# Performance work log

Measured on AMD Instinct MI355X. Metric: run time of the kernel, lower is better.

## Reference

```python
import jax, jax.numpy as jnp
import numpy as np

D_MODEL = 1024
D_HEAD = 64
M_BITS = 32


def setup_inputs() -> dict:
    key = jax.random.key(0)
    ks = jax.random.split(key, 6)
    B, N, M = 2, 2048, 2048
    Q = jax.random.normal(ks[0], (B, N, D_MODEL), dtype=jnp.float32)
    K = jax.random.normal(ks[1], (B, M, D_MODEL), dtype=jnp.float32)
    V = jax.random.normal(ks[2], (B, M, D_MODEL), dtype=jnp.float32)
    s = 1.0 / np.sqrt(D_MODEL)
    Wq = jax.random.normal(ks[3], (D_MODEL, M_BITS), dtype=jnp.float32) * s
    Wk = jax.random.normal(ks[4], (D_MODEL, M_BITS), dtype=jnp.float32) * s
    Wv = jax.random.normal(ks[5], (D_MODEL, D_HEAD), dtype=jnp.float32) * s
    temperature = jnp.ones((1,), dtype=jnp.float32)
    return {"Q": Q, "K": K, "V": V, "Wq": Wq, "Wk": Wk, "Wv": Wv,
            "temperature": temperature}


def tropical_matmul(A, Bt):
    # A: [B, N, m], Bt: [B, M, m] (already transposed form of [B, m, M])
    # (A \odot B)_{ij} = min_k (A_ik + B_kj)
    return jnp.min(A[:, :, None, :] + Bt[:, None, :, :], axis=-1)  # [B, N, M]


def reference(Q, K, V, Wq, Wk, Wv, temperature):
    # REWA tropical encoders (continuous): linear projections to m_bits
    Qt = jnp.einsum('bnd,dm->bnm', Q, Wq)   # [B, N, m_bits]
    Kt = jnp.einsum('bsd,dm->bsm', K, Wk)   # [B, M, m_bits]
    Vp = jnp.einsum('bsd,dh->bsh', V, Wv)   # [B, M, d_head]
    # tropical (min-plus) scores, negated so shorter paths score higher
    scores = -tropical_matmul(Qt, Kt)       # [B, N, M]
    scores = scores / jax.nn.softplus(temperature[0])
    attn = jax.nn.softmax(scores, axis=-1)  # [B, N, M]
    out = jnp.einsum('bnm,bmh->bnh', attn, Vp)  # [B, N, d_head]
    return out, attn
```

## Files before the change

### kernel.cpp

```cpp
#include <hip/hip_runtime.h>
#include <math.h>

#define DM 1024
#define NB 2048
#define MBITS 32
#define DH 64

typedef __attribute__((ext_vector_type(4))) float floatx4;
typedef __attribute__((ext_vector_type(8))) short shortx8;

__device__ __forceinline__ unsigned short f32_to_bf16(float f) {
    union { float f; unsigned u; } v; v.f = f;
    unsigned r = v.u + 0x7FFF + ((v.u >> 16) & 1);
    return (unsigned short)(r >> 16);
}

__device__ __forceinline__ void split2(float x0, float x1, unsigned& hp, unsigned& lp) {
    union { float f; unsigned u; } a, b; a.f = x0; b.f = x1;
    unsigned h0 = a.u & 0xFFFF0000u, h1 = b.u & 0xFFFF0000u;
    union { unsigned u; float f; } hf0, hf1; hf0.u = h0; hf1.u = h1;
    union { float f; unsigned u; } c, d;
    c.f = x0 - hf0.f;
    d.f = x1 - hf1.f;
    hp = (h0 >> 16) | h1;
    lp = (c.u >> 16) | (d.u & 0xFFFF0000u);
}

__global__ __launch_bounds__(256) void wprep_kernel(
    const float* __restrict__ Wq, const float* __restrict__ Wk,
    const float* __restrict__ Wv, unsigned short* __restrict__ Wf)
{
    int wv = blockIdx.x * 4 + (threadIdx.x >> 6);
    int l  = threadIdx.x & 63;
    const float* W; int C, kc32, ct;
    if (wv < 64)       { W = Wq; C = 32; kc32 = wv >> 1;  ct = wv & 1; }
    else if (wv < 128) { W = Wk; C = 32; int z = wv - 64;  kc32 = z >> 1; ct = z & 1; }
    else               { W = Wv; C = 64; int z = wv - 128; kc32 = z >> 2; ct = z & 3; }
    int k0 = kc32 * 32 + (l >> 4) * 8;
    int c  = ct * 16 + (l & 15);
    float x[8];
    #pragma unroll
    for (int j = 0; j < 8; ++j) x[j] = W[(size_t)(k0 + j) * C + c];
    unsigned hp[4], lp[4];
    #pragma unroll
    for (int j2 = 0; j2 < 4; ++j2) split2(x[2 * j2], x[2 * j2 + 1], hp[j2], lp[j2]);
    uint4 hv; hv.x = hp[0]; hv.y = hp[1]; hv.z = hp[2]; hv.w = hp[3];
    uint4 lv; lv.x = lp[0]; lv.y = lp[1]; lv.z = lp[2]; lv.w = lp[3];
    *(uint4*)&Wf[(size_t)wv * 1024 + l * 8]       = hv;
    *(uint4*)&Wf[(size_t)wv * 1024 + 512 + l * 8] = lv;
}

__global__ __launch_bounds__(256) void proj_mfma2_kernel(
    const float* __restrict__ Q, const float* __restrict__ K, const float* __restrict__ V,
    const unsigned short* __restrict__ Wf,
    float* __restrict__ Qt, float* __restrict__ Kt, unsigned short* __restrict__ VpT)
{
    __shared__ float red[4][64][16];

    int gb = blockIdx.x;
    int job = gb >> 8, tile = gb & 255;
    int r0 = tile * 16;
    const float* X = (job == 0) ? Q : (job == 1) ? K : V;
    int ntct  = (job == 2) ? 4 : 2;
    int pbase = job << 6;
    int t = threadIdx.x, w = t >> 6, l = t & 63;
    int lrow = l & 15, lq = l >> 4;

    const float* xrow = &X[(size_t)(r0 + lrow) * DM + w * 256 + lq * 8];

    floatx4 acc[4];
    #pragma unroll
    for (int i = 0; i < 4; ++i) acc[i] = (floatx4){0.f, 0.f, 0.f, 0.f};

    floatx4 g0 = *(const floatx4*)(xrow);
    floatx4 g1 = *(const floatx4*)(xrow + 4);

    #pragma unroll
    for (int s = 0; s < 8; ++s) {
        floatx4 n0, n1;
        if (s < 7) {
            n0 = *(const floatx4*)(xrow + (s + 1) * 32);
            n1 = *(const floatx4*)(xrow + (s + 1) * 32 + 4);
        }
        union { unsigned u[4]; shortx8 v; } ahi, alo;
        split2(g0.x, g0.y, ahi.u[0], alo.u[0]);
        split2(g0.z, g0.w, ahi.u[1], alo.u[1]);
        split2(g1.x, g1.y, ahi.u[2], alo.u[2]);
        split2(g1.z, g1.w, ahi.u[3], alo.u[3]);
        int kc32 = w * 8 + s;
        #pragma unroll
        for (int ct = 0; ct < 4; ++ct) {
            if (ct >= ntct) break;
            int p = pbase + kc32 * ntct + ct;
            const unsigned short* wp = &Wf[(size_t)p * 1024 + l * 8];
            shortx8 bhi = *(const shortx8*)wp;
            shortx8 blo = *(const shortx8*)(wp + 512);
            acc[ct] = __builtin_amdgcn_mfma_f32_16x16x32_bf16(ahi.v, bhi, acc[ct], 0, 0, 0);
            acc[ct] = __builtin_amdgcn_mfma_f32_16x16x32_bf16(ahi.v, blo, acc[ct], 0, 0, 0);
            acc[ct] = __builtin_amdgcn_mfma_f32_16x16x32_bf16(alo.v, bhi, acc[ct], 0, 0, 0);
        }
        g0 = n0; g1 = n1;
    }

    #pragma unroll
    for (int ct = 0; ct < 4; ++ct) {
        if (ct >= ntct) break;
        #pragma unroll
        for (int r = 0; r < 4; ++r) red[w][l][ct * 4 + r] = acc[ct][r];
    }
    __syncthreads();

    int row = r0 + lq * 4 + w;
    if (job < 2) {
        float* Y = (job == 0) ? Qt : Kt;
        #pragma unroll
        for (int ct = 0; ct < 2; ++ct) {
            float v = red[0][l][ct * 4 + w] + red[1][l][ct * 4 + w]
                    + red[2][l][ct * 4 + w] + red[3][l][ct * 4 + w];
            Y[(size_t)row * MBITS + ct * 16 + lrow] = v;
        }
    } else {
        int b = row >> 11, j = row & 2047;
        #pragma unroll
        for (int ct = 0; ct < 4; ++ct) {
            float v = red[0][l][ct * 4 + w] + red[1][l][ct * 4 + w]
                    + red[2][l][ct * 4 + w] + red[3][l][ct * 4 + w];
            VpT[(size_t)b * (DH * NB) + (size_t)(ct * 16 + lrow) * NB + j] = f32_to_bf16(v);
        }
    }
}

__global__ __launch_bounds__(256) void trop_sum_kernel(
    const float* __restrict__ Qt, const float* __restrict__ Kt,
    const float* __restrict__ temp, float* __restrict__ partial)
{
    __shared__ float Qs[16][36];
    __shared__ float Ks[256][36];

    int b  = blockIdx.z;
    int jc = blockIdx.y;
    int i0 = blockIdx.x * 16;
    int t  = threadIdx.x;
    int w  = t >> 6, l = t & 63;

    if (t < 128) {
        int row = t >> 3, k4 = t & 7;
        *(floatx4*)&Qs[row][k4 * 4] =
            *(const floatx4*)&Qt[(size_t)(b * NB + i0 + row) * MBITS + k4 * 4];
    }
    #pragma unroll
    for (int u = 0; u < 8; ++u) {
        int flat4 = u * 256 + t;
        int row = flat4 >> 3, k4 = flat4 & 7;
        *(floatx4*)&Ks[row][k4 * 4] =
            *(const floatx4*)&Kt[(size_t)(b * NB + jc * 256 + row) * MBITS + k4 * 4];
    }
    float tv = temp[0];
    float c2 = -(1.0f / log1pf(__expf(tv))) * 1.44269504088896340736f;
    __syncthreads();

    float m[4][4];
    #pragma unroll
    for (int ii = 0; ii < 4; ++ii)
        #pragma unroll
        for (int jj = 0; jj < 4; ++jj) m[ii][jj] = 1e30f;

    #pragma unroll
    for (int k4 = 0; k4 < 8; ++k4) {
        floatx4 q[4], kk[4];
        #pragma unroll
        for (int ii = 0; ii < 4; ++ii) q[ii] = *(const floatx4*)&Qs[w + 4 * ii][k4 * 4];
        #pragma unroll
        for (int jj = 0; jj < 4; ++jj) kk[jj] = *(const floatx4*)&Ks[l + 64 * jj][k4 * 4];
        #pragma unroll
        for (int ii = 0; ii < 4; ++ii)
            #pragma unroll
            for (int jj = 0; jj < 4; ++jj) {
                float a0 = q[ii].x + kk[jj].x;
                float a1 = q[ii].y + kk[jj].y;
                float a2 = q[ii].z + kk[jj].z;
                float a3 = q[ii].w + kk[jj].w;
                m[ii][jj] = fminf(fminf(m[ii][jj], fminf(a0, a1)), fminf(a2, a3));
            }
    }

    #pragma unroll
    for (int ii = 0; ii < 4; ++ii) {
        float s = exp2f(c2 * m[ii][0]) + exp2f(c2 * m[ii][1])
                + exp2f(c2 * m[ii][2]) + exp2f(c2 * m[ii][3]);
        #pragma unroll
        for (int off = 1; off < 64; off <<= 1) s += __shfl_xor(s, off, 64);
        if (l == 0) partial[((size_t)b * NB + i0 + w + 4 * ii) * 8 + jc] = s;
    }
}

__global__ __launch_bounds__(256) void trop_fused_kernel(
    const float* __restrict__ Qt, const float* __restrict__ Kt,
    const unsigned short* __restrict__ VpT,
    const float* __restrict__ temp, const float* __restrict__ partial,
    float* __restrict__ outp, float* __restrict__ attn)
{
    __shared__ float Qs[16][36];
    __shared__ float Ks[256][36];
    __shared__ unsigned short Es[16][264];
    __shared__ float inv_s[16];

    int b  = blockIdx.z;
    int jc = blockIdx.y;
    int i0 = blockIdx.x * 16;
    int t  = threadIdx.x;
    int w  = t >> 6, l = t & 63;

    if (t < 128) {
        int row = t >> 3, k4 = t & 7;
        *(floatx4*)&Qs[row][k4 * 4] =
            *(const floatx4*)&Qt[(size_t)(b * NB + i0 + row) * MBITS + k4 * 4];
    }
    #pragma unroll
    for (int u = 0; u < 8; ++u) {
        int flat4 = u * 256 + t;
        int row = flat4 >> 3, k4 = flat4 & 7;
        *(floatx4*)&Ks[row][k4 * 4] =
            *(const floatx4*)&Kt[(size_t)(b * NB + jc * 256 + row) * MBITS + k4 * 4];
    }
    if (t < 16) {
        float s = 0.f;
        #pragma unroll
        for (int p = 0; p < 8; ++p) s += partial[((size_t)b * NB + i0 + t) * 8 + p];
        inv_s[t] = 1.0f / s;
    }
    float tv = temp[0];
    float c2 = -(1.0f / log1pf(__expf(tv))) * 1.44269504088896340736f;
    __syncthreads();

    float m[4][4];
    #pragma unroll
    for (int ii = 0; ii < 4; ++ii)
        #pragma unroll
        for (int jj = 0; jj < 4; ++jj) m[ii][jj] = 1e30f;

    #pragma unroll
    for (int k4 = 0; k4 < 8; ++k4) {
        floatx4 q[4], kk[4];
        #pragma unroll
        for (int ii = 0; ii < 4; ++ii) q[ii] = *(const floatx4*)&Qs[w + 4 * ii][k4 * 4];
        #pragma unroll
        for (int jj = 0; jj < 4; ++jj) kk[jj] = *(const floatx4*)&Ks[l + 64 * jj][k4 * 4];
        #pragma unroll
        for (int ii = 0; ii < 4; ++ii)
            #pragma unroll
            for (int jj = 0; jj < 4; ++jj) {
                float a0 = q[ii].x + kk[jj].x;
                float a1 = q[ii].y + kk[jj].y;
                float a2 = q[ii].z + kk[jj].z;
                float a3 = q[ii].w + kk[jj].w;
                m[ii][jj] = fminf(fminf(m[ii][jj], fminf(a0, a1)), fminf(a2, a3));
            }
    }

    #pragma unroll
    for (int ii = 0; ii < 4; ++ii) {
        int i = w + 4 * ii;
        float iv = inv_s[i];
        #pragma unroll
        for (int jj = 0; jj < 4; ++jj) {
            int j = l + 64 * jj;
            float e = exp2f(c2 * m[ii][jj]);
            attn[(size_t)(b * NB + i0 + i) * 2048 + jc * 256 + j] = e * iv;
            Es[i][j] = f32_to_bf16(e);
        }
    }
    __syncthreads();

    const unsigned short* vb =
        &VpT[(size_t)b * (DH * NB) + (size_t)(w * 16 + (l & 15)) * NB
             + jc * 256 + (l >> 4) * 8];
    floatx4 acc = {0.f, 0.f, 0.f, 0.f};
    #pragma unroll
    for (int kk = 0; kk < 8; ++kk) {
        int mrow = l & 15, q4 = l >> 4;
        shortx8 a  = *(const shortx8*)&Es[mrow][kk * 32 + q4 * 8];
        shortx8 bf = *(const shortx8*)(vb + kk * 32);
        acc = __builtin_amdgcn_mfma_f32_16x16x32_bf16(a, bf, acc, 0, 0, 0);
    }

    #pragma unroll
    for (int r = 0; r < 4; ++r) {
        int irow = (l >> 4) * 4 + r;
        atomicAdd(&outp[(size_t)(b * NB + i0 + irow) * DH + w * 16 + (l & 15)],
                  acc[r] * inv_s[irow]);
    }
}

extern "C" void kernel_launch(void* const* d_in, const int* in_sizes, int n_in,
                              void* d_out, int out_size, void* d_ws, size_t ws_size,
                              hipStream_t stream) {
    (void)in_sizes; (void)n_in; (void)out_size; (void)ws_size;
    const float* Q    = (const float*)d_in[0];
    const float* K    = (const float*)d_in[1];
    const float* V    = (const float*)d_in[2];
    const float* Wq   = (const float*)d_in[3];
    const float* Wk   = (const float*)d_in[4];
    const float* Wv   = (const float*)d_in[5];
    const float* temp = (const float*)d_in[6];

    float* outp = (float*)d_out;
    float* attn = outp + 2 * 2048 * 64;

    char* ws = (char*)d_ws;
    float*          Qt      = (float*)(ws);
    float*          Kt      = (float*)(ws + 524288);
    float*          partial = (float*)(ws + 1048576);
    unsigned short* Wf      = (unsigned short*)(ws + 1179648);
    unsigned short* VpT     = (unsigned short*)(ws + 1703936);

    hipMemsetAsync(d_out, 0, 262144 * sizeof(float), stream);

    wprep_kernel<<<64, 256, 0, stream>>>(Wq, Wk, Wv, Wf);
    proj_mfma2_kernel<<<768, 256, 0, stream>>>(Q, K, V, Wf, Qt, Kt, VpT);
    trop_sum_kernel<<<dim3(128, 8, 2), 256, 0, stream>>>(Qt, Kt, temp, partial);
    trop_fused_kernel<<<dim3(128, 8, 2), 256, 0, stream>>>(
        Qt, Kt, VpT, temp, partial, outp, attn);
}
```

Before: 161.2 us.

## Split projection K over 8 waves, swizzle K tiles, replace atomics with partial reduce

The projection kernel now runs 512 threads, with 8 waves each covering half as much of the K dimension, and templates the column-tile count so the inner loop has no branch. In the tropical kernels the padded LDS rows become XOR-swizzled rows, the min chain is rewritten, and the fused kernel reuses the K buffer for the exp tile to cut LDS use. The output atomics and the memset are replaced by per-chunk partial stores plus a separate reduction kernel. The changes trade an extra launch and extra workspace traffic against less contention and better occupancy.

```diff
diff --git a/kernel.cpp b/kernel.cpp
--- a/kernel.cpp
+++ b/kernel.cpp
@@ -50,12 +50,46 @@
     *(uint4*)&Wf[(size_t)wv * 1024 + 512 + l * 8] = lv;
 }
 
-__global__ __launch_bounds__(256) void proj_mfma2_kernel(
+template <int NTCT>
+__device__ __forceinline__ void proj_core(
+    const float* xrow, const unsigned short* __restrict__ Wf,
+    int pbase, int kc32base, int l, floatx4 acc[4])
+{
+    floatx4 g0 = *(const floatx4*)(xrow);
+    floatx4 g1 = *(const floatx4*)(xrow + 4);
+    #pragma unroll
+    for (int s = 0; s < 4; ++s) {
+        floatx4 n0, n1;
+        if (s < 3) {
+            n0 = *(const floatx4*)(xrow + (s + 1) * 32);
+            n1 = *(const floatx4*)(xrow + (s + 1) * 32 + 4);
+        }
+        union { unsigned u[4]; shortx8 v; } ahi, alo;
+        split2(g0.x, g0.y, ahi.u[0], alo.u[0]);
+        split2(g0.z, g0.w, ahi.u[1], alo.u[1]);
+        split2(g1.x, g1.y, ahi.u[2], alo.u[2]);
+        split2(g1.z, g1.w, ahi.u[3], alo.u[3]);
+        int kc32 = kc32base + s;
+        #pragma unroll
+        for (int ct = 0; ct < NTCT; ++ct) {
+            int p = pbase + kc32 * NTCT + ct;
+            const unsigned short* wp = &Wf[(size_t)p * 1024 + l * 8];
+            shortx8 bhi = *(const shortx8*)wp;
+            shortx8 blo = *(const shortx8*)(wp + 512);
+            acc[ct] = __builtin_amdgcn_mfma_f32_16x16x32_bf16(ahi.v, bhi, acc[ct], 0, 0, 0);
+            acc[ct] = __builtin_amdgcn_mfma_f32_16x16x32_bf16(ahi.v, blo, acc[ct], 0, 0, 0);
+            acc[ct] = __builtin_amdgcn_mfma_f32_16x16x32_bf16(alo.v, bhi, acc[ct], 0, 0, 0);
+        }
+        g0 = n0; g1 = n1;
+    }
+}
+
+__global__ __launch_bounds__(512) void proj_mfma3_kernel(
     const float* __restrict__ Q, const float* __restrict__ K, const float* __restrict__ V,
     const unsigned short* __restrict__ Wf,
     float* __restrict__ Qt, float* __restrict__ Kt, unsigned short* __restrict__ VpT)
 {
-    __shared__ float red[4][64][16];
+    __shared__ float red[8][64][17];
 
     int gb = blockIdx.x;
     int job = gb >> 8, tile = gb & 255;
@@ -66,41 +100,14 @@
     int t = threadIdx.x, w = t >> 6, l = t & 63;
     int lrow = l & 15, lq = l >> 4;
 
-    const float* xrow = &X[(size_t)(r0 + lrow) * DM + w * 256 + lq * 8];
+    const float* xrow = &X[(size_t)(r0 + lrow) * DM + w * 128 + lq * 8];
 
     floatx4 acc[4];
     #pragma unroll
     for (int i = 0; i < 4; ++i) acc[i] = (floatx4){0.f, 0.f, 0.f, 0.f};
 
-    floatx4 g0 = *(const floatx4*)(xrow);
-    floatx4 g1 = *(const floatx4*)(xrow + 4);
-
-    #pragma unroll
-    for (int s = 0; s < 8; ++s) {
-        floatx4 n0, n1;
-        if (s < 7) {
-            n0 = *(const floatx4*)(xrow + (s + 1) * 32);
-            n1 = *(const floatx4*)(xrow + (s + 1) * 32 + 4);
-        }
-        union { unsigned u[4]; shortx8 v; } ahi, alo;
-        split2(g0.x, g0.y, ahi.u[0], alo.u[0]);
-        split2(g0.z, g0.w, ahi.u[1], alo.u[1]);
-        split2(g1.x, g1.y, ahi.u[2], alo.u[2]);
-        split2(g1.z, g1.w, ahi.u[3], alo.u[3]);
-        int kc32 = w * 8 + s;
-        #pragma unroll
-        for (int ct = 0; ct < 4; ++ct) {
-            if (ct >= ntct) break;
-            int p = pbase + kc32 * ntct + ct;
-            const unsigned short* wp = &Wf[(size_t)p * 1024 + l * 8];
-            shortx8 bhi = *(const shortx8*)wp;
-            shortx8 blo = *(const shortx8*)(wp + 512);
-            acc[ct] = __builtin_amdgcn_mfma_f32_16x16x32_bf16(ahi.v, bhi, acc[ct], 0, 0, 0);
-            acc[ct] = __builtin_amdgcn_mfma_f32_16x16x32_bf16(ahi.v, blo, acc[ct], 0, 0, 0);
-            acc[ct] = __builtin_amdgcn_mfma_f32_16x16x32_bf16(alo.v, bhi, acc[ct], 0, 0, 0);
-        }
-        g0 = n0; g1 = n1;
-    }
+    if (job < 2) proj_core<2>(xrow, Wf, pbase, w * 4, l, acc);
+    else         proj_core<4>(xrow, Wf, pbase, w * 4, l, acc);
 
     #pragma unroll
     for (int ct = 0; ct < 4; ++ct) {
@@ -110,22 +117,26 @@
     }
     __syncthreads();
 
-    int row = r0 + lq * 4 + w;
-    if (job < 2) {
-        float* Y = (job == 0) ? Qt : Kt;
-        #pragma unroll
-        for (int ct = 0; ct < 2; ++ct) {
-            float v = red[0][l][ct * 4 + w] + red[1][l][ct * 4 + w]
-                    + red[2][l][ct * 4 + w] + red[3][l][ct * 4 + w];
-            Y[(size_t)row * MBITS + ct * 16 + lrow] = v;
-        }
-    } else {
-        int b = row >> 11, j = row & 2047;
-        #pragma unroll
-        for (int ct = 0; ct < 4; ++ct) {
-            float v = red[0][l][ct * 4 + w] + red[1][l][ct * 4 + w]
-                    + red[2][l][ct * 4 + w] + red[3][l][ct * 4 + w];
-            VpT[(size_t)b * (DH * NB) + (size_t)(ct * 16 + lrow) * NB + j] = f32_to_bf16(v);
+    if (w < 4) {
+        int row = r0 + lq * 4 + w;
+        if (job < 2) {
+            float* Y = (job == 0) ? Qt : Kt;
+            #pragma unroll
+            for (int ct = 0; ct < 2; ++ct) {
+                float v = 0.f;
+                #pragma unroll
+                for (int s = 0; s < 8; ++s) v += red[s][l][ct * 4 + w];
+                Y[(size_t)row * MBITS + ct * 16 + lrow] = v;
+            }
+        } else {
+            int b = row >> 11, j = row & 2047;
+            #pragma unroll
+            for (int ct = 0; ct < 4; ++ct) {
+                float v = 0.f;
+                #pragma unroll
+                for (int s = 0; s < 8; ++s) v += red[s][l][ct * 4 + w];
+                VpT[(size_t)b * (DH * NB) + (size_t)(ct * 16 + lrow) * NB + j] = f32_to_bf16(v);
+            }
         }
     }
 }
@@ -134,8 +145,8 @@
     const float* __restrict__ Qt, const float* __restrict__ Kt,
     const float* __restrict__ temp, float* __restrict__ partial)
 {
-    __shared__ float Qs[16][36];
-    __shared__ float Ks[256][36];
+    __shared__ float Qs[16][32];
+    __shared__ float Ks[256][32];
 
     int b  = blockIdx.z;
     int jc = blockIdx.y;
@@ -144,16 +155,16 @@
     int w  = t >> 6, l = t & 63;
 
     if (t < 128) {
-        int row = t >> 3, k4 = t & 7;
-        *(floatx4*)&Qs[row][k4 * 4] =
-            *(const floatx4*)&Qt[(size_t)(b * NB + i0 + row) * MBITS + k4 * 4];
+        int row = t >> 3, c4 = t & 7;
+        *(floatx4*)&Qs[row][c4 * 4] =
+            *(const floatx4*)&Qt[(size_t)(b * NB + i0 + row) * MBITS + c4 * 4];
     }
     #pragma unroll
     for (int u = 0; u < 8; ++u) {
         int flat4 = u * 256 + t;
-        int row = flat4 >> 3, k4 = flat4 & 7;
-        *(floatx4*)&Ks[row][k4 * 4] =
-            *(const floatx4*)&Kt[(size_t)(b * NB + jc * 256 + row) * MBITS + k4 * 4];
+        int row = flat4 >> 3, c4 = flat4 & 7;
+        *(floatx4*)&Ks[row][(c4 ^ (row & 7)) * 4] =
+            *(const floatx4*)&Kt[(size_t)(b * NB + jc * 256 + row) * MBITS + c4 * 4];
     }
     float tv = temp[0];
     float c2 = -(1.0f / log1pf(__expf(tv))) * 1.44269504088896340736f;
@@ -165,22 +176,21 @@
         #pragma unroll
         for (int jj = 0; jj < 4; ++jj) m[ii][jj] = 1e30f;
 
+    int swz = l & 7;
     #pragma unroll
     for (int k4 = 0; k4 < 8; ++k4) {
         floatx4 q[4], kk[4];
         #pragma unroll
         for (int ii = 0; ii < 4; ++ii) q[ii] = *(const floatx4*)&Qs[w + 4 * ii][k4 * 4];
         #pragma unroll
-        for (int jj = 0; jj < 4; ++jj) kk[jj] = *(const floatx4*)&Ks[l + 64 * jj][k4 * 4];
+        for (int jj = 0; jj < 4; ++jj)
+            kk[jj] = *(const floatx4*)&Ks[l + 64 * jj][(k4 ^ swz) * 4];
         #pragma unroll
         for (int ii = 0; ii < 4; ++ii)
             #pragma unroll
             for (int jj = 0; jj < 4; ++jj) {
-                float a0 = q[ii].x + kk[jj].x;
-                float a1 = q[ii].y + kk[jj].y;
-                float a2 = q[ii].z + kk[jj].z;
-                float a3 = q[ii].w + kk[jj].w;
-                m[ii][jj] = fminf(fminf(m[ii][jj], fminf(a0, a1)), fminf(a2, a3));
+                floatx4 av = q[ii] + kk[jj];
+                m[ii][jj] = fminf(fminf(fminf(fminf(m[ii][jj], av.x), av.y), av.z), av.w);
             }
     }
 
@@ -198,12 +208,12 @@
     const float* __restrict__ Qt, const float* __restrict__ Kt,
     const unsigned short* __restrict__ VpT,
     const float* __restrict__ temp, const float* __restrict__ partial,
-    float* __restrict__ outp, float* __restrict__ attn)
-{
-    __shared__ float Qs[16][36];
-    __shared__ float Ks[256][36];
-    __shared__ unsigned short Es[16][264];
+    float* __restrict__ po, float* __restrict__ attn)
+{
+    __shared__ float Qs[16][32];
+    __shared__ float Ks[256][32];
     __shared__ float inv_s[16];
+    unsigned short (*Es)[264] = (unsigned short (*)[264])&Ks[0][0];
 
     int b  = blockIdx.z;
     int jc = blockIdx.y;
@@ -212,16 +222,16 @@
     int w  = t >> 6, l = t & 63;
 
     if (t < 128) {
-        int row = t >> 3, k4 = t & 7;
-        *(floatx4*)&Qs[row][k4 * 4] =
-            *(const floatx4*)&Qt[(size_t)(b * NB + i0 + row) * MBITS + k4 * 4];
+        int row = t >> 3, c4 = t & 7;
+        *(floatx4*)&Qs[row][c4 * 4] =
+            *(const floatx4*)&Qt[(size_t)(b * NB + i0 + row) * MBITS + c4 * 4];
     }
     #pragma unroll
     for (int u = 0; u < 8; ++u) {
         int flat4 = u * 256 + t;
-        int row = flat4 >> 3, k4 = flat4 & 7;
-        *(floatx4*)&Ks[row][k4 * 4] =
-            *(const floatx4*)&Kt[(size_t)(b * NB + jc * 256 + row) * MBITS + k4 * 4];
+        int row = flat4 >> 3, c4 = flat4 & 7;
+        *(floatx4*)&Ks[row][(c4 ^ (row & 7)) * 4] =
+            *(const floatx4*)&Kt[(size_t)(b * NB + jc * 256 + row) * MBITS + c4 * 4];
     }
     if (t < 16) {
         float s = 0.f;
@@ -239,24 +249,24 @@
         #pragma unroll
         for (int jj = 0; jj < 4; ++jj) m[ii][jj] = 1e30f;
 
+    int swz = l & 7;
     #pragma unroll
     for (int k4 = 0; k4 < 8; ++k4) {
         floatx4 q[4], kk[4];
         #pragma unroll
         for (int ii = 0; ii < 4; ++ii) q[ii] = *(const floatx4*)&Qs[w + 4 * ii][k4 * 4];
         #pragma unroll
-        for (int jj = 0; jj < 4; ++jj) kk[jj] = *(const floatx4*)&Ks[l + 64 * jj][k4 * 4];
+        for (int jj = 0; jj < 4; ++jj)
+            kk[jj] = *(const floatx4*)&Ks[l + 64 * jj][(k4 ^ swz) * 4];
         #pragma unroll
         for (int ii = 0; ii < 4; ++ii)
             #pragma unroll
             for (int jj = 0; jj < 4; ++jj) {
-                float a0 = q[ii].x + kk[jj].x;
-                float a1 = q[ii].y + kk[jj].y;
-                float a2 = q[ii].z + kk[jj].z;
-                float a3 = q[ii].w + kk[jj].w;
-                m[ii][jj] = fminf(fminf(m[ii][jj], fminf(a0, a1)), fminf(a2, a3));
+                floatx4 av = q[ii] + kk[jj];
+                m[ii][jj] = fminf(fminf(fminf(fminf(m[ii][jj], av.x), av.y), av.z), av.w);
             }
     }
+    __syncthreads();
 
     #pragma unroll
     for (int ii = 0; ii < 4; ++ii) {
@@ -287,9 +297,20 @@
     #pragma unroll
     for (int r = 0; r < 4; ++r) {
         int irow = (l >> 4) * 4 + r;
-        atomicAdd(&outp[(size_t)(b * NB + i0 + irow) * DH + w * 16 + (l & 15)],
-                  acc[r] * inv_s[irow]);
-    }
+        po[(size_t)jc * 262144 + (size_t)(b * NB + i0 + irow) * DH + w * 16 + (l & 15)] =
+            acc[r] * inv_s[irow];
+    }
+}
+
+__global__ __launch_bounds__(256) void out_reduce_kernel(
+    const float* __restrict__ po, float* __restrict__ outp)
+{
+    int idx4 = (blockIdx.x * 256 + threadIdx.x) * 4;
+    floatx4 a = {0.f, 0.f, 0.f, 0.f};
+    #pragma unroll
+    for (int jc = 0; jc < 8; ++jc)
+        a += *(const floatx4*)&po[(size_t)jc * 262144 + idx4];
+    *(floatx4*)&outp[idx4] = a;
 }
 
 extern "C" void kernel_launch(void* const* d_in, const int* in_sizes, int n_in,
@@ -313,12 +334,12 @@
     float*          partial = (float*)(ws + 1048576);
     unsigned short* Wf      = (unsigned short*)(ws + 1179648);
     unsigned short* VpT     = (unsigned short*)(ws + 1703936);
-
-    hipMemsetAsync(d_out, 0, 262144 * sizeof(float), stream);
+    float*          po      = (float*)(ws + 2228224);
 
     wprep_kernel<<<64, 256, 0, stream>>>(Wq, Wk, Wv, Wf);
-    proj_mfma2_kernel<<<768, 256, 0, stream>>>(Q, K, V, Wf, Qt, Kt, VpT);
+    proj_mfma3_kernel<<<768, 512, 0, stream>>>(Q, K, V, Wf, Qt, Kt, VpT);
     trop_sum_kernel<<<dim3(128, 8, 2), 256, 0, stream>>>(Qt, Kt, temp, partial);
     trop_fused_kernel<<<dim3(128, 8, 2), 256, 0, stream>>>(
-        Qt, Kt, VpT, temp, partial, outp, attn);
-}
+        Qt, Kt, VpT, temp, partial, po, attn);
+    out_reduce_kernel<<<256, 256, 0, stream>>>(po, outp);
+}
```

New measurement: 155.9 us. -3.3%, faster.
